# Optimization experiments

Measured on AMD Instinct MI355X. Metric: run time of the kernel, lower is better.

Reference implementation:

```python
import jax, jax.numpy as jnp
import numpy as np


def _relative_index(ih: int, iw: int) -> np.ndarray:
    # Static precompute mirroring the torch buffer.
    yy, xx = np.meshgrid(np.arange(ih), np.arange(iw), indexing='ij')
    coords = np.stack([yy.ravel(), xx.ravel()])                 # [2, n]
    rel = coords[:, :, None] - coords[:, None, :]               # [2, n, n]
    rel[0] += ih - 1
    rel[1] += iw - 1
    rel[0] *= 2 * iw - 1
    return rel.sum(0).ravel()                                   # [n*n]


def setup_inputs() -> dict:
    key = jax.random.key(0)
    ks = jax.random.split(key, 5)
    B, N, INP, OUP, HEADS = 64, 256, 512, 512, 16
    ih = iw = 16
    return {
        'x': jax.random.normal(ks[0], (B, N, INP), jnp.float32),
        'w_qkv': jax.random.normal(ks[1], (INP, 3 * OUP), jnp.float32) * 0.02,
        'rel_bias_table': jax.random.normal(ks[2], ((2 * ih - 1) * (2 * iw - 1), HEADS), jnp.float32) * 0.02,
        'w_out': jax.random.normal(ks[3], (OUP, OUP), jnp.float32) * 0.02,
        'b_out': jax.random.normal(ks[4], (OUP,), jnp.float32) * 0.02,
        'ih': ih,
        'iw': iw,
    }


def reference(x, w_qkv, rel_bias_table, w_out, b_out, ih, iw):
    B, N, _ = x.shape
    heads = rel_bias_table.shape[1]
    oup = w_out.shape[0]
    dim_head = oup // heads
    scale = dim_head ** -0.5

    qkv = jnp.einsum('bni,ij->bnj', x, w_qkv)                   # [B, N, 3*oup]
    q, k, v = jnp.split(qkv, 3, axis=-1)
    split_heads = lambda t: t.reshape(B, N, heads, dim_head).transpose(0, 2, 1, 3)
    q, k, v = split_heads(q), split_heads(k), split_heads(v)    # [B, H, N, D]

    dots = jnp.einsum('bhnd,bhmd->bhnm', q, k) * scale          # [B, H, N, N]
    rel_idx = jnp.asarray(_relative_index(int(ih), int(iw)))    # [N*N]
    bias = rel_bias_table[rel_idx].reshape(N, N, heads)         # gather
    dots = dots + bias.transpose(2, 0, 1)[None]                 # [1, H, N, N]

    attn = jax.nn.softmax(dots, axis=-1)
    out = jnp.einsum('bhnm,bhmd->bhnd', attn, v)                # [B, H, N, D]
    out = out.transpose(0, 2, 1, 3).reshape(B, N, oup)
    return jnp.einsum('bno,op->bnp', out, w_out.T) + b_out
```

## Files before the change

kernel.cpp:

```cpp
#include <hip/hip_runtime.h>
#include <stdint.h>

typedef unsigned short u16;
typedef unsigned int u32;
typedef __attribute__((ext_vector_type(8))) __bf16 bf16x8;
typedef __attribute__((ext_vector_type(2))) u32 u32x2;
typedef __attribute__((ext_vector_type(4))) u32 u32x4;
typedef __attribute__((ext_vector_type(4))) float f32x4;

__device__ __forceinline__ float bf2f(u16 x) { return __uint_as_float(((u32)x) << 16); }
__device__ __forceinline__ u16 f2bf(float f) {
  u32 u = __float_as_uint(f);
  u32 r = (u + 0x7fffu + ((u >> 16) & 1u)) >> 16;
  return (u16)r;
}
__device__ __forceinline__ u16 cvbf(float f) {
  union { __bf16 b; u16 u; } x;
  x.b = (__bf16)f;
  return x.u;
}

__device__ __forceinline__ u32x2 ld8(const u16* p) { return *(const u32x2*)p; }
__device__ __forceinline__ u32x4 ld16(const u16* p) { return *(const u32x4*)p; }
__device__ __forceinline__ bf16x8 mk_frag(u32x2 lo, u32x2 hi) {
  union { bf16x8 v; u32x2 u[2]; } t;
  t.u[0] = lo; t.u[1] = hi;
  return t.v;
}

__device__ __forceinline__ void stage_fm(u16* lds, int ch, u32x4 v) {
  int row = ch >> 2, q = ch & 3;
  int base = (row >> 4) * 512 + (row & 15) * 8;
  int col0 = q * 8;
  int col1 = q * 8 + 4;
  int d0 = base + (((col0 & 15) >> 2) * 128) + ((col0 >> 4) * 4);
  int d1 = base + (((col1 & 15) >> 2) * 128) + ((col1 >> 4) * 4);
  u32x2 h0; h0.x = v.x; h0.y = v.y;
  u32x2 h1; h1.x = v.z; h1.y = v.w;
  *(u32x2*)&lds[d0] = h0;
  *(u32x2*)&lds[d1] = h1;
}

__device__ __forceinline__ bf16x8 frag_fm(const u16* lds, int subtile, int g, int c) {
  union { bf16x8 v; u32x4 u; } t;
  t.u = ld16(&lds[subtile * 512 + g * 128 + c * 8]);
  return t.v;
}

__global__ void probe_dtype(const u32* __restrict__ x, u32* __restrict__ flag) {
  if (threadIdx.x == 0 && blockIdx.x == 0) {
    int cnt = 0;
    for (int i = 0; i < 32; ++i) {
      u32 e = (x[i] >> 7) & 0xffu;
      cnt += (e >= 96u && e <= 140u) ? 1 : 0;
    }
    *flag = (cnt == 32) ? 1u : 0u;
  }
}

__global__ __launch_bounds__(256) void conv4(const void* __restrict__ src, u16* __restrict__ dst,
                                             const u32* __restrict__ flag, int n4) {
  const bool isbf = (*flag != 0u);
  const int stride = gridDim.x * 256;
  for (int i = blockIdx.x * 256 + threadIdx.x; i < n4; i += stride) {
    if (isbf) {
      ((u32x2*)dst)[i] = ((const u32x2*)src)[i];
    } else {
      const float* s = (const float*)src + (size_t)i * 4;
      u32x2 o;
      o.x = (u32)f2bf(s[0]) | ((u32)f2bf(s[1]) << 16);
      o.y = (u32)f2bf(s[2]) | ((u32)f2bf(s[3]) << 16);
      ((u32x2*)dst)[i] = o;
    }
  }
}

__global__ __launch_bounds__(256) void bias_prep(const void* __restrict__ table,
                                                 float* __restrict__ biasT,
                                                 const u32* __restrict__ flag) {
  const bool isbf = (*flag != 0u);
  int i = blockIdx.x * 256 + threadIdx.x;
  if (i < 16 * 961) {
    int h = i / 961, idx = i - h * 961;
    float v = isbf ? bf2f(((const u16*)table)[idx * 16 + h])
                   : ((const float*)table)[idx * 16 + h];
    biasT[i] = v * 1.4426950408889634f;
  }
}

__global__ __launch_bounds__(256) void transpose_dt(const void* __restrict__ in,
                                                    u16* __restrict__ out,
                                                    const u32* __restrict__ flag, int R, int C) {
  __shared__ u16 t[32][33];
  const bool isbf = (*flag != 0u);
  int r0 = blockIdx.y * 32, c0 = blockIdx.x * 32;
  int rr = threadIdx.x >> 5, cc = threadIdx.x & 31;
#pragma unroll
  for (int i = 0; i < 4; ++i) {
    size_t idx = (size_t)(r0 + rr + i * 8) * C + c0 + cc;
    t[rr + i * 8][cc] = isbf ? ((const u16*)in)[idx] : f2bf(((const float*)in)[idx]);
  }
  __syncthreads();
#pragma unroll
  for (int i = 0; i < 4; ++i) out[(size_t)(c0 + rr + i * 8) * R + r0 + cc] = t[cc][rr + i * 8];
}

__global__ __launch_bounds__(256) void gemm128(const u16* __restrict__ A,
                                               const u16* __restrict__ BT,
                                               u16* __restrict__ O, int K, int ldo) {
  __shared__ u16 As[128 * 32];
  __shared__ u16 Bs[128 * 32];
  const int tid = threadIdx.x;
  const int wave = tid >> 6, lane = tid & 63;
  const int c = lane & 15, g = lane >> 4;
  const int wm = wave >> 1, wn = wave & 1;
  const int bn = blockIdx.x, bm = blockIdx.y;

  const u16* Ab = A + (size_t)bm * 128 * K;
  const u16* Bb = BT + (size_t)bn * 128 * K;

  f32x4 acc[4][4] = {};
  const int row0 = tid >> 2, q0 = tid & 3;
  const int row1 = (tid + 256) >> 2;

  for (int k0 = 0; k0 < K; k0 += 32) {
    u32x4 a0 = ld16(Ab + (size_t)row0 * K + k0 + q0 * 8);
    u32x4 b0 = ld16(Bb + (size_t)row0 * K + k0 + q0 * 8);
    u32x4 a1 = ld16(Ab + (size_t)row1 * K + k0 + q0 * 8);
    u32x4 b1 = ld16(Bb + (size_t)row1 * K + k0 + q0 * 8);
    __syncthreads();
    stage_fm(As, tid, a0);
    stage_fm(Bs, tid, b0);
    stage_fm(As, tid + 256, a1);
    stage_fm(Bs, tid + 256, b1);
    __syncthreads();
    bf16x8 af[4], bfr[4];
#pragma unroll
    for (int i = 0; i < 4; ++i) {
      af[i] = frag_fm(As, wm * 4 + i, g, c);
      bfr[i] = frag_fm(Bs, wn * 4 + i, g, c);
    }
#pragma unroll
    for (int i = 0; i < 4; ++i)
#pragma unroll
      for (int j = 0; j < 4; ++j)
        acc[i][j] = __builtin_amdgcn_mfma_f32_16x16x32_bf16(af[i], bfr[j], acc[i][j], 0, 0, 0);
  }

#pragma unroll
  for (int i = 0; i < 4; ++i)
#pragma unroll
    for (int j = 0; j < 4; ++j) {
      int jg = bn * 128 + wn * 64 + j * 16 + c;
#pragma unroll
      for (int r = 0; r < 4; ++r) {
        int mg = bm * 128 + wm * 64 + i * 16 + 4 * g + r;
        O[(size_t)mg * ldo + jg] = f2bf(acc[i][j][r]);
      }
    }
}

__global__ __launch_bounds__(256) void gemm_final(const u16* __restrict__ A,
                                                  const u16* __restrict__ BT,
                                                  const u16* __restrict__ bias,
                                                  void* __restrict__ O, int row0g,
                                                  const u32* __restrict__ flag) {
  __shared__ u16 As[128 * 32];
  __shared__ u16 Bs[128 * 32];
  const int K = 512;
  const bool isbf = (*flag != 0u);
  const int tid = threadIdx.x;
  const int wave = tid >> 6, lane = tid & 63;
  const int c = lane & 15, g = lane >> 4;
  const int wm = wave >> 1, wn = wave & 1;
  const int bn = blockIdx.x, bm = blockIdx.y;

  const u16* Ab = A + (size_t)bm * 128 * K;
  const u16* Bb = BT + (size_t)bn * 128 * K;

  f32x4 acc[4][4] = {};
  const int row0 = tid >> 2, q0 = tid & 3;
  const int row1 = (tid + 256) >> 2;

  for (int k0 = 0; k0 < K; k0 += 32) {
    u32x4 a0 = ld16(Ab + (size_t)row0 * K + k0 + q0 * 8);
    u32x4 b0 = ld16(Bb + (size_t)row0 * K + k0 + q0 * 8);
    u32x4 a1 = ld16(Ab + (size_t)row1 * K + k0 + q0 * 8);
    u32x4 b1 = ld16(Bb + (size_t)row1 * K + k0 + q0 * 8);
    __syncthreads();
    stage_fm(As, tid, a0);
    stage_fm(Bs, tid, b0);
    stage_fm(As, tid + 256, a1);
    stage_fm(Bs, tid + 256, b1);
    __syncthreads();
    bf16x8 af[4], bfr[4];
#pragma unroll
    for (int i = 0; i < 4; ++i) {
      af[i] = frag_fm(As, wm * 4 + i, g, c);
      bfr[i] = frag_fm(Bs, wn * 4 + i, g, c);
    }
#pragma unroll
    for (int i = 0; i < 4; ++i)
#pragma unroll
      for (int j = 0; j < 4; ++j)
        acc[i][j] = __builtin_amdgcn_mfma_f32_16x16x32_bf16(af[i], bfr[j], acc[i][j], 0, 0, 0);
  }

#pragma unroll
  for (int i = 0; i < 4; ++i)
#pragma unroll
    for (int j = 0; j < 4; ++j) {
      int jg = bn * 128 + wn * 64 + j * 16 + c;
      float bv = bf2f(bias[jg]);
#pragma unroll
      for (int r = 0; r < 4; ++r) {
        int mg = bm * 128 + wm * 64 + i * 16 + 4 * g + r;
        float v = acc[i][j][r] + bv;
        size_t off = (size_t)(row0g + mg) * 512 + jg;
        if (isbf) ((u16*)O)[off] = f2bf(v);
        else ((float*)O)[off] = v;
      }
    }
}

__global__ __launch_bounds__(256) void attn_kernel(const u16* __restrict__ qkv,
                                                   const float* __restrict__ biasT,
                                                   u16* __restrict__ Out) {
  __shared__ u16 smem[18432];
  float* biasS = (float*)&smem[16384];

  const int tid = threadIdx.x;
  const int wave = tid >> 6, lane = tid & 63;
  const int c = lane & 15, g = lane >> 4;
  const int half = blockIdx.x & 1;
  const int h = (blockIdx.x >> 1) & 15;
  const int b = blockIdx.x >> 5;

  const u16* xb = qkv + (size_t)b * 256 * 1536;

  u32x4 kvr[4];
#pragma unroll
  for (int i = 0; i < 4; ++i) {
    int ch = tid + i * 256;
    int m = ch >> 2;
    kvr[i] = ld16(xb + (size_t)m * 1536 + 512 + h * 32 + (ch & 3) * 8);
  }
#pragma unroll
  for (int i = 0; i < 4; ++i) stage_fm(smem, tid + i * 256, kvr[i]);

#pragma unroll
  for (int i = 0; i < 16; ++i) {
    int e2 = tid + i * 256;
    int n = e2 >> 4, d = (e2 & 15) * 2;
    u32 val = *(const u32*)(xb + (size_t)n * 1536 + 1024 + h * 32 + d);
    smem[8192 + d * 256 + (n ^ (8 * (d & 7)))] = (u16)(val & 0xffffu);
    smem[8192 + (d + 1) * 256 + (n ^ (8 * ((d + 1) & 7)))] = (u16)(val >> 16);
  }
  for (int i = tid; i < 961; i += 256) biasS[i] = biasT[h * 961 + i];

  u32x2 qlo[2], qhi[2];
#pragma unroll
  for (int rg = 0; rg < 2; ++rg) {
    const u16* qp = xb + (size_t)((half * 2 + rg) * 64 + wave * 16 + c) * 1536 + h * 32 + 4 * g;
    qlo[rg] = ld8(qp);
    qhi[rg] = ld8(qp + 16);
  }
  __syncthreads();

  const u16* Vt = &smem[8192];
  const int va = 8 * (c & 7);
  const float scale2 = 0.25503484f;
  const float* bp0 = biasS + wave * 31 + c + 12 - 4 * g;

#pragma unroll
  for (int rg = 0; rg < 2; ++rg) {
    const int rgg = half * 2 + rg;
    bf16x8 qf = mk_frag(qlo[rg], qhi[rg]);

    f32x4 o0 = {0.f, 0.f, 0.f, 0.f}, o1 = {0.f, 0.f, 0.f, 0.f};
    float smm = 0.f;

#pragma unroll
    for (int ph = 0; ph < 2; ++ph) {
      f32x4 s[8];
#pragma unroll
      for (int f = 0; f < 8; ++f) {
        bf16x8 kf = frag_fm(smem, ph * 8 + f, g, c);
        f32x4 z = {0.f, 0.f, 0.f, 0.f};
        s[f] = __builtin_amdgcn_mfma_f32_16x16x32_bf16(kf, qf, z, 0, 0, 0);
      }

      float u[8];
#pragma unroll
      for (int f = 0; f < 8; ++f) {
        const int fg = ph * 8 + f;
#pragma unroll
        for (int j = 0; j < 4; ++j) {
          float bv = bp0[(rgg * 4 - fg + 15) * 31 + 3 - j];
          s[f][j] = __builtin_amdgcn_exp2f(s[f][j] * scale2 + bv);
        }
        u[f] = (s[f][0] + s[f][1]) + (s[f][2] + s[f][3]);
      }
      smm += ((u[0] + u[4]) + (u[1] + u[5])) + ((u[2] + u[6]) + (u[3] + u[7]));

#pragma unroll
      for (int q = 0; q < 4; ++q) {
        bf16x8 pf;
        pf[0] = (__bf16)s[2 * q][0]; pf[1] = (__bf16)s[2 * q][1];
        pf[2] = (__bf16)s[2 * q][2]; pf[3] = (__bf16)s[2 * q][3];
        pf[4] = (__bf16)s[2 * q + 1][0]; pf[5] = (__bf16)s[2 * q + 1][1];
        pf[6] = (__bf16)s[2 * q + 1][2]; pf[7] = (__bf16)s[2 * q + 1][3];
        const int kg = (ph * 4 + q) * 32;
        bf16x8 v0 = mk_frag(ld8(&Vt[c * 256 + ((kg + 4 * g) ^ va)]),
                            ld8(&Vt[c * 256 + ((kg + 16 + 4 * g) ^ va)]));
        bf16x8 v1 = mk_frag(ld8(&Vt[(16 + c) * 256 + ((kg + 4 * g) ^ va)]),
                            ld8(&Vt[(16 + c) * 256 + ((kg + 16 + 4 * g) ^ va)]));
        o0 = __builtin_amdgcn_mfma_f32_16x16x32_bf16(pf, v0, o0, 0, 0, 0);
        o1 = __builtin_amdgcn_mfma_f32_16x16x32_bf16(pf, v1, o1, 0, 0, 0);
      }
    }

    smm += __shfl_xor(smm, 16, 64);
    smm += __shfl_xor(smm, 32, 64);
    const float invc = __builtin_amdgcn_rcpf(smm);

    const int nb = rgg * 64 + wave * 16 + 4 * g;
#pragma unroll
    for (int j = 0; j < 4; ++j) {
      int n = nb + j;
      size_t off = ((size_t)b * 256 + n) * 512 + h * 32;
      Out[off + c] = cvbf(o0[j] * invc);
      Out[off + 16 + c] = cvbf(o1[j] * invc);
    }
  }
}

extern "C" void kernel_launch(void* const* d_in, const int* in_sizes, int n_in, void* d_out,
                              int out_size, void* d_ws, size_t ws_size, hipStream_t stream) {
  (void)in_sizes; (void)n_in; (void)out_size;
  const void* x = d_in[0];
  const void* w_qkv = d_in[1];
  const void* table = d_in[2];
  const void* w_out = d_in[3];
  const void* b_out = d_in[4];

  char* ws = (char*)d_ws;
  u32* flag = (u32*)ws;
  u16* xc = (u16*)(ws + 256);
  u16* wqkvT = (u16*)(ws + 16777472);
  float* biasT = (float*)(ws + 18350336);
  u16* woC = (u16*)(ws + 18411840);
  u16* bC = (u16*)(ws + 18936128);
  const size_t DYN = 18937344;
  int CB = 64;
  while (CB > 1 && DYN + (size_t)CB * 1048576 > ws_size) CB >>= 1;
  u16* qkv = (u16*)(ws + DYN);
  u16* att = (u16*)(ws + DYN + (size_t)CB * 786432);

  dim3 blk(256);
  probe_dtype<<<dim3(1), dim3(64), 0, stream>>>((const u32*)x, flag);
  conv4<<<dim3(2048), blk, 0, stream>>>(x, xc, flag, 2097152);
  conv4<<<dim3(256), blk, 0, stream>>>(w_out, woC, flag, 65536);
  conv4<<<dim3(1), blk, 0, stream>>>(b_out, bC, flag, 128);
  bias_prep<<<dim3(61), blk, 0, stream>>>(table, biasT, flag);
  transpose_dt<<<dim3(48, 16), blk, 0, stream>>>(w_qkv, wqkvT, flag, 512, 1536);

  for (int s0 = 0; s0 < 64; s0 += CB) {
    const u16* xcc = xc + (size_t)s0 * 256 * 512;
    gemm128<<<dim3(12, CB * 2), blk, 0, stream>>>(xcc, wqkvT, qkv, 512, 1536);
    attn_kernel<<<dim3(CB * 32), blk, 0, stream>>>(qkv, biasT, att);
    gemm_final<<<dim3(4, CB * 2), blk, 0, stream>>>(att, woC, bC, d_out, s0 * 256, flag);
  }
}
```

Baseline: 133.0 us.

## Stage GEMM tiles via direct global-to-LDS loads with contiguous k layout

Replaces register-staged global loads plus scattered LDS writes in both GEMM kernels with global_load_lds 16-byte direct transfers. The LDS tile layout changes to a contiguous 8-element k chunk per lane, so the attention kernel's K staging and Q fragment loads now use single 16-byte accesses. This is consistent because the k permutation is applied to both operands. The intent is to remove VGPR round-trips and LDS write instructions, at the cost of an extra barrier per k-iteration.

```diff
diff --git a/kernel.cpp b/kernel.cpp
--- a/kernel.cpp
+++ b/kernel.cpp
@@ -28,17 +28,15 @@
   return t.v;
 }
 
+__device__ __forceinline__ void g2l16(const void* g, void* l) {
+  __builtin_amdgcn_global_load_lds(
+      (const __attribute__((address_space(1))) u32*)g,
+      (__attribute__((address_space(3))) u32*)l, 16, 0, 0);
+}
+
 __device__ __forceinline__ void stage_fm(u16* lds, int ch, u32x4 v) {
   int row = ch >> 2, q = ch & 3;
-  int base = (row >> 4) * 512 + (row & 15) * 8;
-  int col0 = q * 8;
-  int col1 = q * 8 + 4;
-  int d0 = base + (((col0 & 15) >> 2) * 128) + ((col0 >> 4) * 4);
-  int d1 = base + (((col1 & 15) >> 2) * 128) + ((col1 >> 4) * 4);
-  u32x2 h0; h0.x = v.x; h0.y = v.y;
-  u32x2 h1; h1.x = v.z; h1.y = v.w;
-  *(u32x2*)&lds[d0] = h0;
-  *(u32x2*)&lds[d1] = h1;
+  *(u32x4*)&lds[(row >> 4) * 512 + q * 128 + (row & 15) * 8] = v;
 }
 
 __device__ __forceinline__ bf16x8 frag_fm(const u16* lds, int subtile, int g, int c) {
@@ -119,20 +117,20 @@
   const u16* Ab = A + (size_t)bm * 128 * K;
   const u16* Bb = BT + (size_t)bn * 128 * K;
 
+  const u16* Arow = Ab + (size_t)(wave * 16 + c) * K + 8 * g;
+  const u16* Brow = Bb + (size_t)(wave * 16 + c) * K + 8 * g;
+  u16* Ad0 = &As[wave * 512 + lane * 8];
+  u16* Ad1 = &As[(wave + 4) * 512 + lane * 8];
+  u16* Bd0 = &Bs[wave * 512 + lane * 8];
+  u16* Bd1 = &Bs[(wave + 4) * 512 + lane * 8];
+
   f32x4 acc[4][4] = {};
-  const int row0 = tid >> 2, q0 = tid & 3;
-  const int row1 = (tid + 256) >> 2;
 
   for (int k0 = 0; k0 < K; k0 += 32) {
-    u32x4 a0 = ld16(Ab + (size_t)row0 * K + k0 + q0 * 8);
-    u32x4 b0 = ld16(Bb + (size_t)row0 * K + k0 + q0 * 8);
-    u32x4 a1 = ld16(Ab + (size_t)row1 * K + k0 + q0 * 8);
-    u32x4 b1 = ld16(Bb + (size_t)row1 * K + k0 + q0 * 8);
-    __syncthreads();
-    stage_fm(As, tid, a0);
-    stage_fm(Bs, tid, b0);
-    stage_fm(As, tid + 256, a1);
-    stage_fm(Bs, tid + 256, b1);
+    g2l16(Arow + k0, Ad0);
+    g2l16(Arow + 64 * K + k0, Ad1);
+    g2l16(Brow + k0, Bd0);
+    g2l16(Brow + 64 * K + k0, Bd1);
     __syncthreads();
     bf16x8 af[4], bfr[4];
 #pragma unroll
@@ -145,6 +143,7 @@
 #pragma unroll
       for (int j = 0; j < 4; ++j)
         acc[i][j] = __builtin_amdgcn_mfma_f32_16x16x32_bf16(af[i], bfr[j], acc[i][j], 0, 0, 0);
+    __syncthreads();
   }
 
 #pragma unroll
@@ -178,20 +177,20 @@
   const u16* Ab = A + (size_t)bm * 128 * K;
   const u16* Bb = BT + (size_t)bn * 128 * K;
 
+  const u16* Arow = Ab + (size_t)(wave * 16 + c) * K + 8 * g;
+  const u16* Brow = Bb + (size_t)(wave * 16 + c) * K + 8 * g;
+  u16* Ad0 = &As[wave * 512 + lane * 8];
+  u16* Ad1 = &As[(wave + 4) * 512 + lane * 8];
+  u16* Bd0 = &Bs[wave * 512 + lane * 8];
+  u16* Bd1 = &Bs[(wave + 4) * 512 + lane * 8];
+
   f32x4 acc[4][4] = {};
-  const int row0 = tid >> 2, q0 = tid & 3;
-  const int row1 = (tid + 256) >> 2;
 
   for (int k0 = 0; k0 < K; k0 += 32) {
-    u32x4 a0 = ld16(Ab + (size_t)row0 * K + k0 + q0 * 8);
-    u32x4 b0 = ld16(Bb + (size_t)row0 * K + k0 + q0 * 8);
-    u32x4 a1 = ld16(Ab + (size_t)row1 * K + k0 + q0 * 8);
-    u32x4 b1 = ld16(Bb + (size_t)row1 * K + k0 + q0 * 8);
-    __syncthreads();
-    stage_fm(As, tid, a0);
-    stage_fm(Bs, tid, b0);
-    stage_fm(As, tid + 256, a1);
-    stage_fm(Bs, tid + 256, b1);
+    g2l16(Arow + k0, Ad0);
+    g2l16(Arow + 64 * K + k0, Ad1);
+    g2l16(Brow + k0, Bd0);
+    g2l16(Brow + 64 * K + k0, Bd1);
     __syncthreads();
     bf16x8 af[4], bfr[4];
 #pragma unroll
@@ -204,6 +203,7 @@
 #pragma unroll
       for (int j = 0; j < 4; ++j)
         acc[i][j] = __builtin_amdgcn_mfma_f32_16x16x32_bf16(af[i], bfr[j], acc[i][j], 0, 0, 0);
+    __syncthreads();
   }
 
 #pragma unroll
@@ -258,12 +258,11 @@
   }
   for (int i = tid; i < 961; i += 256) biasS[i] = biasT[h * 961 + i];
 
-  u32x2 qlo[2], qhi[2];
+  u32x4 qv[2];
 #pragma unroll
   for (int rg = 0; rg < 2; ++rg) {
-    const u16* qp = xb + (size_t)((half * 2 + rg) * 64 + wave * 16 + c) * 1536 + h * 32 + 4 * g;
-    qlo[rg] = ld8(qp);
-    qhi[rg] = ld8(qp + 16);
+    const u16* qp = xb + (size_t)((half * 2 + rg) * 64 + wave * 16 + c) * 1536 + h * 32 + 8 * g;
+    qv[rg] = ld16(qp);
   }
   __syncthreads();
 
@@ -275,7 +274,9 @@
 #pragma unroll
   for (int rg = 0; rg < 2; ++rg) {
     const int rgg = half * 2 + rg;
-    bf16x8 qf = mk_frag(qlo[rg], qhi[rg]);
+    union { bf16x8 v; u32x4 u; } qt;
+    qt.u = qv[rg];
+    bf16x8 qf = qt.v;
 
     f32x4 o0 = {0.f, 0.f, 0.f, 0.f}, o1 = {0.f, 0.f, 0.f, 0.f};
     float smm = 0.f;
```

Measured after the change: 150.6 us. 13.2% more time.
